# Kernel optimization log

Hardware: AMD Instinct MI355X
Metric: run time of the kernel (lower is better)

The kernel has to match this reference:

```python
import jax, jax.numpy as jnp
import numpy as np

ACT_BIT = 8
WEIGHT_BIT = 8
GELU_K = 1.4142
GELU_CONST = 14
C0, C1 = -0.2888, -1.769
C2 = 1.0 / C0  # coeff[2] /= coeff[0]


def round_ste(x):
    return x + jax.lax.stop_gradient(jnp.round(x) - x)


def floor_ste(x):
    return x + jax.lax.stop_gradient(jnp.floor(x) - x)


def sym_scale(bit, smin, smax):
    # symmetric_linear_quantization_params
    n = 2 ** (bit - 1) - 1
    return jnp.clip(jnp.maximum(jnp.abs(smin), jnp.abs(smax)), 1e-8, None) / n


def quant_linear(x, sf_in, weight, bias):
    # per-channel symmetric int8 weight quant, int32 bias, scaled int GEMM
    n = 2 ** (WEIGHT_BIT - 1) - 1
    w_sf = sym_scale(WEIGHT_BIT, weight.min(axis=1), weight.max(axis=1))  # [O]
    w_int = jnp.clip(round_ste(weight / w_sf[:, None]), -n - 1, n)       # [O,H]
    bias_sf = w_sf * sf_in                                               # [O]
    b_int = round_ste(bias / bias_sf)
    x_int = x / sf_in                                                    # [B,S,H]
    out_int = jnp.einsum('bsh,oh->bso', x_int, w_int) + b_int
    return out_int * bias_sf, bias_sf


def int_gelu(x, sf):
    # integer polynomial erf approximation (I-BERT IntGELU)
    x_int = x / sf
    sf_e = sf / GELU_K
    b_int = jnp.floor(C1 / sf_e)
    c_int = jnp.floor(C2 / sf_e ** 2)
    sign = jnp.sign(x_int)
    abs_int = jnp.minimum(jnp.abs(x_int), -b_int)
    y_int = sign * ((abs_int + b_int) ** 2 + c_int)
    sf_sig = sf_e ** 2 * C0
    y_int = floor_ste(y_int / 2.0 ** GELU_CONST)
    sf_sig = sf_sig * 2 ** GELU_CONST
    shift_int = jnp.floor(1.0 / sf_sig)
    x_int = x_int * (y_int + shift_int)
    sf_out = sf * sf_sig / 2
    return x_int * sf_out, sf_out


def quant_act(x, pre_sf):
    # QuantAct: requantize to 8 bits via dyadic (frexp) fixed-point multiply
    n = 2 ** (ACT_BIT - 1) - 1
    sf = sym_scale(ACT_BIT, x.min(), x.max())  # scalar
    z_int = jnp.round(x / pre_sf)
    m, e = jnp.frexp(pre_sf / sf)              # pre_sf is per-channel [O]
    m_int = jnp.round(m * 2.0 ** 31)
    out_int = jnp.clip(jnp.round(z_int * m_int / 2.0 ** (31 - e)), -n - 1, n)
    # FixedPointMul backward is identity w.r.t. x (straight-through)
    q_int = x + jax.lax.stop_gradient(out_int - x)
    return q_int * sf, sf


def setup_inputs() -> dict:
    key = jax.random.key(0)
    k1, k2, k3 = jax.random.split(key, 3)
    B, S, H, I = 8, 2048, 1024, 4096
    sf = jnp.array([0.02], dtype=jnp.float32)
    x = jax.random.normal(k1, (B, S, H), dtype=jnp.float32)
    # pre-quantized 8-bit activations on the incoming grid
    x = jnp.clip(jnp.round(x / sf) * sf, -128 * 0.02, 127 * 0.02)
    weight = jax.random.normal(k2, (I, H), dtype=jnp.float32) * 0.02
    bias = jax.random.normal(k3, (I,), dtype=jnp.float32) * 0.01
    return {"hidden_states": x, "hidden_states_scaling_factor": sf,
            "weight": weight, "bias": bias}


def reference(hidden_states, hidden_states_scaling_factor, weight, bias):
    h, sf = quant_linear(hidden_states, hidden_states_scaling_factor, weight, bias)
    h, sf = int_gelu(h, sf)
    h, sf = quant_act(h, sf)
    return h, sf
```

## Files before the change

kernel.cpp:

```cpp
#include <hip/hip_runtime.h>

#define M_TOK 16384
#define K_DIM 1024
#define N_DIM 4096
#define SLABA ((size_t)M_TOK * 64)
#define SLABB ((size_t)N_DIM * 64)

using i32x4 = __attribute__((ext_vector_type(4))) int;

__device__ __forceinline__ float gelu_q(int acc, float4 pa, float4 pb) {
  float oi = (float)acc + pa.x;
  float h  = oi * pa.y;
  float xi = h / pa.y;
  float sgn = (xi > 0.f) ? 1.f : ((xi < 0.f) ? -1.f : 0.f);
  float ab  = fminf(fabsf(xi), -pa.z);
  float tt  = ab + pa.z;
  float yi  = sgn * (tt * tt + pa.w);
  yi = floorf(yi * (1.0f / 16384.0f));
  return xi * (yi + pb.x);
}

__global__ void k_prep_x(const float* __restrict__ x,
                         const float* __restrict__ sfp,
                         char* __restrict__ x8) {
  float r = 1.0f / sfp[0];
  int i4 = blockIdx.x * 256 + threadIdx.x;
  float4 v = ((const float4*)x)[i4];
  int c0 = (int)rintf(v.x * r);
  int c1 = (int)rintf(v.y * r);
  int c2 = (int)rintf(v.z * r);
  int c3 = (int)rintf(v.w * r);
  int packed = (c0 & 0xFF) | ((c1 & 0xFF) << 8) | ((c2 & 0xFF) << 16)
             | ((c3 & 0xFF) << 24);
  int m = i4 >> 8, kq = i4 & 255;
  ((int*)(x8 + (size_t)(kq >> 4) * SLABA + (size_t)m * 64))[kq & 15] = packed;
}

__global__ void k_prep_w(const float* __restrict__ W,
                         const float* __restrict__ bias,
                         const float* __restrict__ sfp,
                         char* __restrict__ w8,
                         float4* __restrict__ cA,
                         float4* __restrict__ cB) {
  const int o = blockIdx.x;
  const int t = threadIdx.x;
  float4 wv = ((const float4*)(W + (size_t)o * K_DIM))[t];
  float vmn = fminf(fminf(wv.x, wv.y), fminf(wv.z, wv.w));
  float vmx = fmaxf(fmaxf(wv.x, wv.y), fmaxf(wv.z, wv.w));
#pragma unroll
  for (int off = 32; off; off >>= 1) {
    vmn = fminf(vmn, __shfl_down(vmn, off, 64));
    vmx = fmaxf(vmx, __shfl_down(vmx, off, 64));
  }
  __shared__ float sm[8];
  __shared__ float s_wsf;
  int lane = t & 63, wv_id = t >> 6;
  if (lane == 0) { sm[wv_id] = vmn; sm[4 + wv_id] = vmx; }
  __syncthreads();
  if (t == 0) {
    float mn = fminf(fminf(sm[0], sm[1]), fminf(sm[2], sm[3]));
    float mx = fmaxf(fmaxf(sm[4], sm[5]), fmaxf(sm[6], sm[7]));
    float wsf = fmaxf(fmaxf(fabsf(mn), fabsf(mx)), 1e-8f) / 127.0f;
    s_wsf = wsf;
    float sfin = sfp[0];
    float bsf  = wsf * sfin;
    float bint = rintf(bias[o] / bsf);
    float sfe  = bsf / 1.4142f;
    float bg   = floorf(-1.769f / sfe);
    const float C2F = (float)(1.0 / -0.2888);
    float cg   = floorf(C2F / (sfe * sfe));
    float sfsig = sfe * sfe * (-0.2888f);
    sfsig = sfsig * 16384.0f;
    float shiftint = floorf(1.0f / sfsig);
    float sfout = bsf * sfsig / 2.0f;
    cA[o] = make_float4(bint, bsf, bg, cg);
    cB[o] = make_float4(shiftint, sfout, 0.0f, 0.0f);
  }
  __syncthreads();
  float wsf = s_wsf;
  int q0 = (int)fminf(fmaxf(rintf(wv.x / wsf), -128.f), 127.f);
  int q1 = (int)fminf(fmaxf(rintf(wv.y / wsf), -128.f), 127.f);
  int q2 = (int)fminf(fmaxf(rintf(wv.z / wsf), -128.f), 127.f);
  int q3 = (int)fminf(fmaxf(rintf(wv.w / wsf), -128.f), 127.f);
  int packed = (q0 & 0xFF) | ((q1 & 0xFF) << 8) | ((q2 & 0xFF) << 16)
             | ((q3 & 0xFF) << 24);
  ((int*)(w8 + (size_t)(t >> 4) * SLABB + (size_t)o * 64))[t & 15] = packed;
}

__global__ __launch_bounds__(256) void k_gemm(
    const char* __restrict__ A, const char* __restrict__ B,
    const float4* __restrict__ cA, const float4* __restrict__ cB,
    float* __restrict__ out, float2* __restrict__ pmm) {
  const int t = threadIdx.x;
  const int lane = t & 63;
  const int w = t >> 6;
  const int wm = w >> 1, wn = w & 1;
  const int m0 = blockIdx.y * 128;
  const int n0 = blockIdx.x * 128;
  const int fr = lane & 15;
  const int loff = fr * 64 + (lane >> 4) * 16;

  const char* Ap = A + (size_t)(m0 + wm * 64) * 64 + loff;
  const char* Bp = B + (size_t)(n0 + wn * 64) * 64 + loff;

  i32x4 acc[4][4] = {};
  i32x4 a0[4], b0[4], a1[4], b1[4];
#pragma unroll
  for (int i = 0; i < 4; ++i) {
    a0[i] = *(const i32x4*)(Ap + i * 1024);
    b0[i] = *(const i32x4*)(Bp + i * 1024);
  }
#pragma unroll 2
  for (int it = 0; it < K_DIM / 64; ++it) {
    if (it + 1 < K_DIM / 64) {
#pragma unroll
      for (int i = 0; i < 4; ++i) {
        a1[i] = *(const i32x4*)(Ap + (it + 1) * SLABA + i * 1024);
        b1[i] = *(const i32x4*)(Bp + (it + 1) * SLABB + i * 1024);
      }
    }
#pragma unroll
    for (int mi = 0; mi < 4; ++mi)
#pragma unroll
      for (int ni = 0; ni < 4; ++ni)
        acc[mi][ni] = __builtin_amdgcn_mfma_i32_16x16x64_i8(
            a0[mi], b0[ni], acc[mi][ni], 0, 0, 0);
#pragma unroll
    for (int i = 0; i < 4; ++i) { a0[i] = a1[i]; b0[i] = b1[i]; }
  }

  const int rowb = m0 + wm * 64 + (lane >> 4) * 4;
  const int colb = n0 + wn * 64 + fr;
  float vmin = 3.4e38f, vmax = -3.4e38f;

#pragma unroll
  for (int ni = 0; ni < 4; ++ni) {
    const int col = colb + ni * 16;
    const float4 pa = cA[col];
    const float4 pb = cB[col];
#pragma unroll
    for (int mi = 0; mi < 4; ++mi) {
#pragma unroll
      for (int r = 0; r < 4; ++r) {
        float q  = gelu_q(acc[mi][ni][r], pa, pb);
        float xg = q * pb.y;
        vmin = fminf(vmin, xg);
        vmax = fmaxf(vmax, xg);
        out[(size_t)(rowb + mi * 16 + r) * N_DIM + col] = q;
      }
    }
  }

#pragma unroll
  for (int off = 32; off; off >>= 1) {
    vmin = fminf(vmin, __shfl_down(vmin, off, 64));
    vmax = fmaxf(vmax, __shfl_down(vmax, off, 64));
  }
  __shared__ float swmn[4], swmx[4];
  if (lane == 0) { swmn[w] = vmin; swmx[w] = vmax; }
  __syncthreads();
  if (t == 0) {
    float bmn = fminf(fminf(swmn[0], swmn[1]), fminf(swmn[2], swmn[3]));
    float bmx = fmaxf(fmaxf(swmx[0], swmx[1]), fmaxf(swmx[2], swmx[3]));
    pmm[blockIdx.y * gridDim.x + blockIdx.x] = make_float2(bmn, bmx);
  }
}

__global__ void k_scalar(const float2* __restrict__ pmm,
                         const float4* __restrict__ cB,
                         float* __restrict__ cR,
                         float* __restrict__ sfws,
                         float* __restrict__ out_sf) {
  const int t = threadIdx.x;
  float mn = 3.4e38f, mx = -3.4e38f;
  for (int i = t; i < 4096; i += 256) {
    float2 p = pmm[i];
    mn = fminf(mn, p.x);
    mx = fmaxf(mx, p.y);
  }
#pragma unroll
  for (int off = 32; off; off >>= 1) {
    mn = fminf(mn, __shfl_down(mn, off, 64));
    mx = fmaxf(mx, __shfl_down(mx, off, 64));
  }
  __shared__ float sm[8];
  __shared__ float s_sf;
  int lane = t & 63, wid = t >> 6;
  if (lane == 0) { sm[wid] = mn; sm[4 + wid] = mx; }
  __syncthreads();
  if (t == 0) {
    float m0 = fminf(fminf(sm[0], sm[1]), fminf(sm[2], sm[3]));
    float m1 = fmaxf(fmaxf(sm[4], sm[5]), fmaxf(sm[6], sm[7]));
    float sf = fmaxf(fmaxf(fabsf(m0), fabsf(m1)), 1e-8f) / 127.0f;
    s_sf = sf;
    if (blockIdx.x == 0) { sfws[0] = sf; out_sf[0] = sf; }
  }
  __syncthreads();
  float sf = s_sf;
  int o = blockIdx.x * 256 + t;
  float psf = cB[o].y;
  int e;
  float mm = frexpf(psf / sf, &e);
  float mi = rintf(mm * 2147483648.0f);
  cR[o] = mi * ldexpf(1.0f, e - 31);
}

__global__ __launch_bounds__(256) void k_requant(
    float* __restrict__ out, const float* __restrict__ cR,
    const float* __restrict__ sfws) {
  const float sf = sfws[0];
  size_t i4 = (size_t)blockIdx.x * 256 + threadIdx.x;
  float4 v = ((const float4*)out)[i4];
  int col4 = (int)(i4 & (N_DIM / 4 - 1));
  float4 c = ((const float4*)cR)[col4];
  v.x = fminf(fmaxf(rintf(rintf(v.x) * c.x), -128.f), 127.f) * sf;
  v.y = fminf(fmaxf(rintf(rintf(v.y) * c.y), -128.f), 127.f) * sf;
  v.z = fminf(fmaxf(rintf(rintf(v.z) * c.z), -128.f), 127.f) * sf;
  v.w = fminf(fmaxf(rintf(rintf(v.w) * c.w), -128.f), 127.f) * sf;
  ((float4*)out)[i4] = v;
}

extern "C" void kernel_launch(void* const* d_in, const int* in_sizes, int n_in,
                              void* d_out, int out_size, void* d_ws, size_t ws_size,
                              hipStream_t stream) {
  const float* x    = (const float*)d_in[0];
  const float* sfp  = (const float*)d_in[1];
  const float* W    = (const float*)d_in[2];
  const float* bias = (const float*)d_in[3];
  float* out = (float*)d_out;

  char* ws = (char*)d_ws;
  char* x8 = ws;
  char* w8 = ws + (size_t)M_TOK * K_DIM;
  char* tail = ws + (size_t)M_TOK * K_DIM + (size_t)N_DIM * K_DIM;
  float4* cA = (float4*)tail;
  float4* cB = (float4*)(tail + (size_t)N_DIM * 16);
  float* cR  = (float*)(tail + (size_t)N_DIM * 32);
  float2* pmm = (float2*)(tail + (size_t)N_DIM * 36);
  float* sfws = (float*)(tail + (size_t)N_DIM * 36 + 32768);

  k_prep_x<<<(M_TOK * K_DIM / 4) / 256, 256, 0, stream>>>(x, sfp, x8);
  k_prep_w<<<N_DIM, 256, 0, stream>>>(W, bias, sfp, w8, cA, cB);
  k_gemm<<<dim3(N_DIM / 128, M_TOK / 128), 256, 0, stream>>>(
      x8, w8, cA, cB, out, pmm);
  k_scalar<<<N_DIM / 256, 256, 0, stream>>>(pmm, cB, cR, sfws,
                                            out + (size_t)M_TOK * N_DIM);
  k_requant<<<(M_TOK * N_DIM / 4) / 256, 256, 0, stream>>>(out, cR, sfws);
}
```

Before: 534.9 us.

## Add nontemporal memory ops, XCD-aware tile remap, and ping-pong GEMM prefetch

Several independent changes. Streaming loads and stores become nontemporal in the x prep, the GEMM epilogue and the requant pass. GEMM tiles are remapped so that blocks on the same XCD share column tiles for L2 reuse. The K loop is manually double-buffered with two register sets so the register copies go away. The gelu drops a redundant multiply and divide by the scale, min/max is taken on the integer result before scaling per column, and requant becomes grid-stride with a fixed grid. Dropping the multiply-divide and moving the min/max before scaling can change rounding slightly.

```diff
diff --git a/kernel.cpp b/kernel.cpp
--- a/kernel.cpp
+++ b/kernel.cpp
@@ -7,11 +7,10 @@
 #define SLABB ((size_t)N_DIM * 64)
 
 using i32x4 = __attribute__((ext_vector_type(4))) int;
+using f32x4 = __attribute__((ext_vector_type(4))) float;
 
 __device__ __forceinline__ float gelu_q(int acc, float4 pa, float4 pb) {
-  float oi = (float)acc + pa.x;
-  float h  = oi * pa.y;
-  float xi = h / pa.y;
+  float xi = (float)acc + pa.x;
   float sgn = (xi > 0.f) ? 1.f : ((xi < 0.f) ? -1.f : 0.f);
   float ab  = fminf(fabsf(xi), -pa.z);
   float tt  = ab + pa.z;
@@ -25,7 +24,7 @@
                          char* __restrict__ x8) {
   float r = 1.0f / sfp[0];
   int i4 = blockIdx.x * 256 + threadIdx.x;
-  float4 v = ((const float4*)x)[i4];
+  f32x4 v = __builtin_nontemporal_load((const f32x4*)x + i4);
   int c0 = (int)rintf(v.x * r);
   int c1 = (int)rintf(v.y * r);
   int c2 = (int)rintf(v.z * r);
@@ -95,8 +94,15 @@
   const int lane = t & 63;
   const int w = t >> 6;
   const int wm = w >> 1, wn = w & 1;
-  const int m0 = blockIdx.y * 128;
-  const int n0 = blockIdx.x * 128;
+
+  const int lin = blockIdx.y * gridDim.x + blockIdx.x;
+  const int xcd = lin & 7;
+  const int local = lin >> 3;
+  const int bx = xcd * 4 + (local & 3);
+  const int by = local >> 2;
+  const int m0 = by * 128;
+  const int n0 = bx * 128;
+
   const int fr = lane & 15;
   const int loff = fr * 64 + (lane >> 4) * 16;
 
@@ -104,19 +110,30 @@
   const char* Bp = B + (size_t)(n0 + wn * 64) * 64 + loff;
 
   i32x4 acc[4][4] = {};
-  i32x4 a0[4], b0[4], a1[4], b1[4];
+  i32x4 ax[4], bxr[4], ay[4], byr[4];
 #pragma unroll
   for (int i = 0; i < 4; ++i) {
-    a0[i] = *(const i32x4*)(Ap + i * 1024);
-    b0[i] = *(const i32x4*)(Bp + i * 1024);
-  }
-#pragma unroll 2
-  for (int it = 0; it < K_DIM / 64; ++it) {
-    if (it + 1 < K_DIM / 64) {
+    ax[i]  = *(const i32x4*)(Ap + i * 1024);
+    bxr[i] = *(const i32x4*)(Bp + i * 1024);
+  }
+#pragma unroll
+  for (int it = 0; it < K_DIM / 64; it += 2) {
+#pragma unroll
+    for (int i = 0; i < 4; ++i) {
+      ay[i]  = *(const i32x4*)(Ap + (size_t)(it + 1) * SLABA + i * 1024);
+      byr[i] = *(const i32x4*)(Bp + (size_t)(it + 1) * SLABB + i * 1024);
+    }
+#pragma unroll
+    for (int mi = 0; mi < 4; ++mi)
+#pragma unroll
+      for (int ni = 0; ni < 4; ++ni)
+        acc[mi][ni] = __builtin_amdgcn_mfma_i32_16x16x64_i8(
+            ax[mi], bxr[ni], acc[mi][ni], 0, 0, 0);
+    if (it + 2 < K_DIM / 64) {
 #pragma unroll
       for (int i = 0; i < 4; ++i) {
-        a1[i] = *(const i32x4*)(Ap + (it + 1) * SLABA + i * 1024);
-        b1[i] = *(const i32x4*)(Bp + (it + 1) * SLABB + i * 1024);
+        ax[i]  = *(const i32x4*)(Ap + (size_t)(it + 2) * SLABA + i * 1024);
+        bxr[i] = *(const i32x4*)(Bp + (size_t)(it + 2) * SLABB + i * 1024);
       }
     }
 #pragma unroll
@@ -124,9 +141,7 @@
 #pragma unroll
       for (int ni = 0; ni < 4; ++ni)
         acc[mi][ni] = __builtin_amdgcn_mfma_i32_16x16x64_i8(
-            a0[mi], b0[ni], acc[mi][ni], 0, 0, 0);
-#pragma unroll
-    for (int i = 0; i < 4; ++i) { a0[i] = a1[i]; b0[i] = b1[i]; }
+            ay[mi], byr[ni], acc[mi][ni], 0, 0, 0);
   }
 
   const int rowb = m0 + wm * 64 + (lane >> 4) * 4;
@@ -138,17 +153,21 @@
     const int col = colb + ni * 16;
     const float4 pa = cA[col];
     const float4 pb = cB[col];
+    float qmn = 3.4e38f, qmx = -3.4e38f;
 #pragma unroll
     for (int mi = 0; mi < 4; ++mi) {
 #pragma unroll
       for (int r = 0; r < 4; ++r) {
-        float q  = gelu_q(acc[mi][ni][r], pa, pb);
-        float xg = q * pb.y;
-        vmin = fminf(vmin, xg);
-        vmax = fmaxf(vmax, xg);
-        out[(size_t)(rowb + mi * 16 + r) * N_DIM + col] = q;
+        float q = gelu_q(acc[mi][ni][r], pa, pb);
+        qmn = fminf(qmn, q);
+        qmx = fmaxf(qmx, q);
+        __builtin_nontemporal_store(
+            q, &out[(size_t)(rowb + mi * 16 + r) * N_DIM + col]);
       }
     }
+    float xa = qmn * pb.y, xb = qmx * pb.y;
+    vmin = fminf(vmin, fminf(xa, xb));
+    vmax = fmaxf(vmax, fmaxf(xa, xb));
   }
 
 #pragma unroll
@@ -162,7 +181,7 @@
   if (t == 0) {
     float bmn = fminf(fminf(swmn[0], swmn[1]), fminf(swmn[2], swmn[3]));
     float bmx = fmaxf(fmaxf(swmx[0], swmx[1]), fmaxf(swmx[2], swmx[3]));
-    pmm[blockIdx.y * gridDim.x + blockIdx.x] = make_float2(bmn, bmx);
+    pmm[lin] = make_float2(bmn, bmx);
   }
 }
 
@@ -209,15 +228,18 @@
     float* __restrict__ out, const float* __restrict__ cR,
     const float* __restrict__ sfws) {
   const float sf = sfws[0];
-  size_t i4 = (size_t)blockIdx.x * 256 + threadIdx.x;
-  float4 v = ((const float4*)out)[i4];
-  int col4 = (int)(i4 & (N_DIM / 4 - 1));
-  float4 c = ((const float4*)cR)[col4];
-  v.x = fminf(fmaxf(rintf(rintf(v.x) * c.x), -128.f), 127.f) * sf;
-  v.y = fminf(fmaxf(rintf(rintf(v.y) * c.y), -128.f), 127.f) * sf;
-  v.z = fminf(fmaxf(rintf(rintf(v.z) * c.z), -128.f), 127.f) * sf;
-  v.w = fminf(fmaxf(rintf(rintf(v.w) * c.w), -128.f), 127.f) * sf;
-  ((float4*)out)[i4] = v;
+  const size_t n4 = (size_t)M_TOK * N_DIM / 4;
+  for (size_t i4 = (size_t)blockIdx.x * 256 + threadIdx.x; i4 < n4;
+       i4 += (size_t)gridDim.x * 256) {
+    f32x4 v = __builtin_nontemporal_load((const f32x4*)out + i4);
+    int col4 = (int)(i4 & (N_DIM / 4 - 1));
+    float4 c = ((const float4*)cR)[col4];
+    v.x = fminf(fmaxf(rintf(rintf(v.x) * c.x), -128.f), 127.f) * sf;
+    v.y = fminf(fmaxf(rintf(rintf(v.y) * c.y), -128.f), 127.f) * sf;
+    v.z = fminf(fmaxf(rintf(rintf(v.z) * c.z), -128.f), 127.f) * sf;
+    v.w = fminf(fmaxf(rintf(rintf(v.w) * c.w), -128.f), 127.f) * sf;
+    __builtin_nontemporal_store(v, (f32x4*)out + i4);
+  }
 }
 
 extern "C" void kernel_launch(void* const* d_in, const int* in_sizes, int n_in,
@@ -245,5 +267,5 @@
       x8, w8, cA, cB, out, pmm);
   k_scalar<<<N_DIM / 256, 256, 0, stream>>>(pmm, cB, cR, sfws,
                                             out + (size_t)M_TOK * N_DIM);
-  k_requant<<<(M_TOK * N_DIM / 4) / 256, 256, 0, stream>>>(out, cR, sfws);
-}
+  k_requant<<<8192, 256, 0, stream>>>(out, cR, sfws);
+}
```

Result: no change. 542.1 us (+1.4%).
